# Optimization experiments

Hardware: AMD Instinct MI355X
Metric: run time of the kernel (lower is better)

## Reference

```python
import jax, jax.numpy as jnp
import numpy as np

B, T, C = 512, 256, 384
HEAD = 64

def setup_inputs() -> dict:
    key = jax.random.key(0)
    k1, k2, k3, k4 = jax.random.split(key, 4)
    x = jax.random.normal(k1, (B, T, C), dtype=jnp.float32)
    Wq = jax.random.normal(k2, (C, HEAD), dtype=jnp.float32) * (C ** -0.5)
    Wk = jax.random.normal(k3, (C, HEAD), dtype=jnp.float32) * (C ** -0.5)
    Wv = jax.random.normal(k4, (C, HEAD), dtype=jnp.float32) * (C ** -0.5)
    return {"x": x, "Wq": Wq, "Wk": Wk, "Wv": Wv}

def reference(x, Wq, Wk, Wv):
    # projections (Linear with bias=False): x @ W
    q = jnp.einsum('btc,ch->bth', x, Wq)   # [B,T,H]
    k = jnp.einsum('btc,ch->bth', x, Wk)   # [B,T,H]
    v = jnp.einsum('btc,ch->bth', x, Wv)   # [B,T,H]
    Cdim = x.shape[-1]
    # NOTE: original scales by C**-0.5 where C = nEmbd (not headSize)
    scores = jnp.einsum('bth,bsh->bts', q, k) * (Cdim ** -0.5)  # [B,T,T]
    Tlen = x.shape[1]
    causal = jnp.tril(jnp.ones((Tlen, Tlen), dtype=bool))
    scores = jnp.where(causal, scores, -jnp.inf)
    wei = jax.nn.softmax(scores, axis=-1)
    # dropout omitted (eval mode / deterministic reference)
    out = jnp.einsum('bts,bsh->bth', wei, v)  # [B,T,H]
    return out
```

## Files before the change

### kernel.cpp

```cpp
#include <hip/hip_runtime.h>

#define B_ 512
#define T_ 256
#define C_ 384
#define H_ 64

typedef __bf16 bf16;
typedef bf16  bf16x8 __attribute__((ext_vector_type(8)));
typedef bf16  bf16x2 __attribute__((ext_vector_type(2)));
typedef float f32x4  __attribute__((ext_vector_type(4)));
typedef int   i32x4  __attribute__((ext_vector_type(4)));

#define NCHUNK     3
#define CHUNK_K    128
#define WT3_CHUNK  24576
#define WT3_TOTAL  (NCHUNK * WT3_CHUNK)

__global__ void prep_wt3(const float* __restrict__ Wq,
                         const float* __restrict__ Wk,
                         const float* __restrict__ Wv,
                         bf16* __restrict__ wt3)
{
    int idx = blockIdx.x * 256 + threadIdx.x;
    if (idx >= WT3_TOTAL) return;
    int chunk = idx / WT3_CHUNK;
    int rem   = idx % WT3_CHUNK;
    int s     = rem >> 3;
    int e     = rem & 7;
    int mc    = s >> 4;
    int kkc   = (s & 15) ^ (mc & 7);
    int mat   = mc >> 6;
    int col   = mc & 63;
    int k     = chunk * CHUNK_K + kkc * 8 + e;
    const float* W = (mat == 0) ? Wq : (mat == 1) ? Wk : Wv;
    wt3[idx] = (bf16)W[k * H_ + col];
}

__device__ __forceinline__ bf16x8 cvt8(float4 a, float4 b)
{
    bf16x8 r;
    r[0] = (bf16)a.x; r[1] = (bf16)a.y; r[2] = (bf16)a.z; r[3] = (bf16)a.w;
    r[4] = (bf16)b.x; r[5] = (bf16)b.y; r[6] = (bf16)b.z; r[7] = (bf16)b.w;
    return r;
}

__device__ __forceinline__ unsigned pack2(float a, float b)
{
    bf16x2 v; v[0] = (bf16)a; v[1] = (bf16)b;
    return __builtin_bit_cast(unsigned, v);
}

__device__ __forceinline__ void gload_lds16(const bf16* g, bf16* l)
{
    __builtin_amdgcn_global_load_lds(
        (const __attribute__((address_space(1))) void*)g,
        (__attribute__((address_space(3))) void*)l,
        16, 0, 0);
}

#define SWZ(row, col) ((col) ^ (((row) & 7) << 3))

__device__ __forceinline__ const bf16x8* wts_frag(const bf16* wt_s, int mc, int kk)
{
    int byte = ((mc * CHUNK_K + kk) * 2) ^ ((mc & 7) << 4);
    return reinterpret_cast<const bf16x8*>(reinterpret_cast<const char*>(wt_s) + byte);
}

template<int USE_WT>
__global__ __launch_bounds__(512, 2)
void head_fused12(const float* __restrict__ x,
                  const float* __restrict__ Wq,
                  const float* __restrict__ Wk,
                  const float* __restrict__ Wv,
                  const bf16* __restrict__ wt3,
                  float* __restrict__ out)
{
    __shared__ bf16 lds_u[32768];
    __shared__ bf16 p_s[8 * 16 * 64];

    bf16* wt_s = lds_u;
    bf16* k_s  = lds_u;
    bf16* vT_s = lds_u + 16384;

    const int tid  = threadIdx.x;
    const int wave = tid >> 6;
    const int lane = tid & 63;
    const int lr   = lane & 15;
    const int lg   = lane >> 4;

    const int b = blockIdx.x;
    const float* xb = x + (size_t)b * T_ * C_;
    bf16* pw = &p_s[wave * 16 * 64];

    const int mt0 = wave, mt1 = 15 - wave;
    bf16x8 qf[2][2];

    f32x4 acc[2][3][4];
    #pragma unroll
    for (int t = 0; t < 2; ++t)
        #pragma unroll
        for (int a = 0; a < 3; ++a)
            #pragma unroll
            for (int nw = 0; nw < 4; ++nw)
                acc[t][a][nw] = (f32x4){0.f, 0.f, 0.f, 0.f};

    #pragma unroll 1
    for (int chunk = 0; chunk < NCHUNK; ++chunk) {
        if (chunk) __syncthreads();
        if (USE_WT) {
            #pragma unroll
            for (int c = 0; c < 6; ++c) {
                const bf16* g = wt3 + chunk * WT3_CHUNK + (c * 512 + tid) * 8;
                bf16* l = wt_s + (c * 512 + wave * 64) * 8;
                gload_lds16(g, l);
            }
        } else {
            #pragma unroll
            for (int c = 0; c < 6; ++c) {
                int f16 = c * 512 + tid;
                int mc  = f16 >> 4;
                int kkc = f16 & 15;
                int mat = mc >> 6, col = mc & 63;
                const float* W = (mat == 0) ? Wq : (mat == 1) ? Wk : Wv;
                bf16x8 vv;
                #pragma unroll
                for (int j = 0; j < 8; ++j)
                    vv[j] = (bf16)W[(chunk * CHUNK_K + kkc * 8 + j) * H_ + col];
                int byte = ((mc * CHUNK_K + kkc * 8) * 2) ^ ((mc & 7) << 4);
                *reinterpret_cast<bf16x8*>(reinterpret_cast<char*>(wt_s) + byte) = vv;
            }
        }
        __syncthreads();

        const float* xr0 = xb + (mt0 * 16 + lr) * C_ + chunk * CHUNK_K + lg * 8;
        const float* xr1 = xb + (mt1 * 16 + lr) * C_ + chunk * CHUNK_K + lg * 8;
        #pragma unroll
        for (int ks = 0; ks < 4; ++ks) {
            float4 a0 = *reinterpret_cast<const float4*>(xr0 + ks * 32);
            float4 a1 = *reinterpret_cast<const float4*>(xr0 + ks * 32 + 4);
            float4 b0 = *reinterpret_cast<const float4*>(xr1 + ks * 32);
            float4 b1 = *reinterpret_cast<const float4*>(xr1 + ks * 32 + 4);
            bf16x8 af0 = cvt8(a0, a1);
            bf16x8 af1 = cvt8(b0, b1);
            const int kk = ks * 32 + lg * 8;
            #pragma unroll
            for (int mat = 0; mat < 3; ++mat) {
                #pragma unroll
                for (int nw = 0; nw < 4; ++nw) {
                    bf16x8 bfr = *wts_frag(wt_s, mat * 64 + nw * 16 + lr, kk);
                    acc[0][mat][nw] = __builtin_amdgcn_mfma_f32_16x16x32_bf16(
                        af0, bfr, acc[0][mat][nw], 0, 0, 0);
                    acc[1][mat][nw] = __builtin_amdgcn_mfma_f32_16x16x32_bf16(
                        af1, bfr, acc[1][mat][nw], 0, 0, 0);
                }
            }
        }
    }
    __syncthreads();

    #pragma unroll
    for (int tile = 0; tile < 2; ++tile) {
        const int mt = tile ? mt1 : mt0;
        #pragma unroll
        for (int nw = 0; nw < 4; ++nw) {
            #pragma unroll
            for (int r = 0; r < 4; ++r) {
                int row = mt * 16 + lg * 4 + r;
                int col = nw * 16 + lr;
                k_s[row * 64 + SWZ(row, col)]   = (bf16)acc[tile][1][nw][r];
                vT_s[col * 256 + SWZ(col, row)] = (bf16)acc[tile][2][nw][r];
            }
        }
        #pragma unroll
        for (int nw = 0; nw < 4; ++nw) {
            #pragma unroll
            for (int r = 0; r < 4; ++r) {
                int row = lg * 4 + r;
                pw[row * 64 + SWZ(row, nw * 16 + lr)] = (bf16)acc[tile][0][nw][r];
            }
        }
        asm volatile("s_waitcnt lgkmcnt(0)" ::: "memory");
        __builtin_amdgcn_sched_barrier(0);
        qf[tile][0] = *reinterpret_cast<const bf16x8*>(&pw[lr * 64 + SWZ(lr, lg * 8)]);
        qf[tile][1] = *reinterpret_cast<const bf16x8*>(&pw[lr * 64 + SWZ(lr, 32 + lg * 8)]);
        asm volatile("s_waitcnt lgkmcnt(0)" ::: "memory");
        __builtin_amdgcn_sched_barrier(0);
    }
    __syncthreads();

    const float scale = 0.051031036307982884f;

    #pragma unroll
    for (int p = 0; p < 2; ++p) {
        const int mt  = p ? mt1 : mt0;
        const int nkt = mt + 1;

        float m = -1e30f, l = 0.f;
        f32x4 oacc[4];
        #pragma unroll
        for (int n = 0; n < 4; ++n) oacc[n] = (f32x4){0.f, 0.f, 0.f, 0.f};

        #pragma unroll
        for (int h = 0; h < 2; ++h) {
            const int vh = (nkt - h * 8) < 8 ? (nkt - h * 8) : 8;
            if (vh > 0) {
                float s[8][4];
                #pragma unroll
                for (int j = 0; j < 8; ++j) {
                    const int kt = h * 8 + j;
                    if (j < vh) {
                        bf16x8 kf0 = *reinterpret_cast<const bf16x8*>(
                            &k_s[(kt * 16 + lr) * 64 + SWZ(lr, lg * 8)]);
                        bf16x8 kf1 = *reinterpret_cast<const bf16x8*>(
                            &k_s[(kt * 16 + lr) * 64 + SWZ(lr, 32 + lg * 8)]);
                        f32x4 sc = (f32x4){0.f, 0.f, 0.f, 0.f};
                        sc = __builtin_amdgcn_mfma_f32_16x16x32_bf16(kf0, qf[p][0], sc, 0, 0, 0);
                        sc = __builtin_amdgcn_mfma_f32_16x16x32_bf16(kf1, qf[p][1], sc, 0, 0, 0);
                        #pragma unroll
                        for (int r = 0; r < 4; ++r) {
                            float v = sc[r] * scale;
                            if (kt == mt && (lg * 4 + r) > lr) v = -1e30f;
                            s[j][r] = v;
                        }
                    } else {
                        #pragma unroll
                        for (int r = 0; r < 4; ++r) s[j][r] = -1e30f;
                    }
                }

                float pm = s[0][0];
                #pragma unroll
                for (int j = 0; j < 8; ++j)
                    #pragma unroll
                    for (int r = 0; r < 4; ++r) pm = fmaxf(pm, s[j][r]);
                pm = fmaxf(pm, __shfl_xor(pm, 16));
                pm = fmaxf(pm, __shfl_xor(pm, 32));
                float nm = fmaxf(m, pm);
                float fr = __expf(m - nm);
                m = nm;
                l *= fr;
                #pragma unroll
                for (int n = 0; n < 4; ++n)
                    #pragma unroll
                    for (int r = 0; r < 4; ++r) oacc[n][r] *= fr;

                float tt = 0.f;
                #pragma unroll
                for (int j = 0; j < 8; ++j)
                    #pragma unroll
                    for (int r = 0; r < 4; ++r) {
                        float e = __expf(s[j][r] - m);
                        s[j][r] = e;
                        tt += e;
                    }
                tt += __shfl_xor(tt, 16);
                tt += __shfl_xor(tt, 32);
                l += tt;

                const int nkk = (vh + 1) >> 1;
                #pragma unroll
                for (int kkl = 0; kkl < 4; ++kkl) {
                    if (kkl < nkk) {
                        const int kk = h * 4 + kkl;
                        unsigned lo0 = pack2(s[2*kkl][0],   s[2*kkl][1]);
                        unsigned hi0 = pack2(s[2*kkl][2],   s[2*kkl][3]);
                        unsigned lo1 = pack2(s[2*kkl+1][0], s[2*kkl+1][1]);
                        unsigned hi1 = pack2(s[2*kkl+1][2], s[2*kkl+1][3]);
                        const int src0 = (lg & 1) * 32 + lr;
                        const int src1 = src0 + 16;
                        const bool t1  = (lg >> 1) != 0;
                        int a0 = __shfl((int)lo0, src0), a1 = __shfl((int)lo1, src0);
                        unsigned w0 = t1 ? (unsigned)a1 : (unsigned)a0;
                        int b0 = __shfl((int)hi0, src0), b1 = __shfl((int)hi1, src0);
                        unsigned w1 = t1 ? (unsigned)b1 : (unsigned)b0;
                        int c0 = __shfl((int)lo0, src1), c1 = __shfl((int)lo1, src1);
                        unsigned w2 = t1 ? (unsigned)c1 : (unsigned)c0;
                        int d0 = __shfl((int)hi0, src1), d1 = __shfl((int)hi1, src1);
                        unsigned w3 = t1 ? (unsigned)d1 : (unsigned)d0;
                        i32x4 wi = {(int)w0, (int)w1, (int)w2, (int)w3};
                        bf16x8 pf = __builtin_bit_cast(bf16x8, wi);
                        #pragma unroll
                        for (int n = 0; n < 4; ++n) {
                            bf16x8 vf = *reinterpret_cast<const bf16x8*>(
                                &vT_s[(n * 16 + lr) * 256 + SWZ(lr, kk * 32 + lg * 8)]);
                            oacc[n] = __builtin_amdgcn_mfma_f32_16x16x32_bf16(vf, pf, oacc[n], 0, 0, 0);
                        }
                    }
                }
            }
        }

        const float rin = 1.0f / l;
        float* op = out + ((size_t)b * T_ + mt * 16 + lr) * H_;
        #pragma unroll
        for (int n = 0; n < 4; ++n) {
            float4 st;
            st.x = oacc[n][0] * rin;
            st.y = oacc[n][1] * rin;
            st.z = oacc[n][2] * rin;
            st.w = oacc[n][3] * rin;
            *reinterpret_cast<float4*>(op + n * 16 + lg * 4) = st;
        }
    }
}

extern "C" void kernel_launch(void* const* d_in, const int* in_sizes, int n_in,
                              void* d_out, int out_size, void* d_ws, size_t ws_size,
                              hipStream_t stream)
{
    (void)in_sizes; (void)n_in; (void)out_size;
    const float* x  = (const float*)d_in[0];
    const float* Wq = (const float*)d_in[1];
    const float* Wk = (const float*)d_in[2];
    const float* Wv = (const float*)d_in[3];
    float* o = (float*)d_out;

    if (ws_size >= (size_t)(WT3_TOTAL * sizeof(bf16))) {
        bf16* wt3 = (bf16*)d_ws;
        prep_wt3<<<dim3((WT3_TOTAL + 255) / 256), dim3(256), 0, stream>>>(Wq, Wk, Wv, wt3);
        head_fused12<1><<<dim3(B_), dim3(512), 0, stream>>>(x, Wq, Wk, Wv, wt3, o);
    } else {
        head_fused12<0><<<dim3(B_), dim3(512), 0, stream>>>(x, Wq, Wk, Wv, nullptr, o);
    }
}
```

Before: 64.91 us.

## Double-buffer weight chunks in LDS to overlap staging with projection MFMAs

Splits the K dimension of the QKV projection into six 64-wide chunks and ping-pongs two LDS weight buffers. The next chunk's weight load is issued before the current chunk's MFMAs, so global-to-LDS traffic overlaps compute. This removes one of the two barriers per chunk. In exchange there are twice as many chunk iterations and barriers, and the x reads per iteration are smaller.

```diff
diff --git a/kernel.cpp b/kernel.cpp
--- a/kernel.cpp
+++ b/kernel.cpp
@@ -11,9 +11,9 @@
 typedef float f32x4  __attribute__((ext_vector_type(4)));
 typedef int   i32x4  __attribute__((ext_vector_type(4)));
 
-#define NCHUNK     3
-#define CHUNK_K    128
-#define WT3_CHUNK  24576
+#define NCHUNK     6
+#define CHUNK_K    64
+#define WT3_CHUNK  12288
 #define WT3_TOTAL  (NCHUNK * WT3_CHUNK)
 
 __global__ void prep_wt3(const float* __restrict__ Wq,
@@ -27,8 +27,8 @@
     int rem   = idx % WT3_CHUNK;
     int s     = rem >> 3;
     int e     = rem & 7;
-    int mc    = s >> 4;
-    int kkc   = (s & 15) ^ (mc & 7);
+    int mc    = s >> 3;
+    int kkc   = (s & 7) ^ (mc & 7);
     int mat   = mc >> 6;
     int col   = mc & 63;
     int k     = chunk * CHUNK_K + kkc * 8 + e;
@@ -60,15 +60,15 @@
 
 #define SWZ(row, col) ((col) ^ (((row) & 7) << 3))
 
-__device__ __forceinline__ const bf16x8* wts_frag(const bf16* wt_s, int mc, int kk)
+__device__ __forceinline__ const bf16x8* wts_frag(const bf16* buf, int mc, int kk)
 {
     int byte = ((mc * CHUNK_K + kk) * 2) ^ ((mc & 7) << 4);
-    return reinterpret_cast<const bf16x8*>(reinterpret_cast<const char*>(wt_s) + byte);
+    return reinterpret_cast<const bf16x8*>(reinterpret_cast<const char*>(buf) + byte);
 }
 
 template<int USE_WT>
 __global__ __launch_bounds__(512, 2)
-void head_fused12(const float* __restrict__ x,
+void head_fused13(const float* __restrict__ x,
                   const float* __restrict__ Wq,
                   const float* __restrict__ Wk,
                   const float* __restrict__ Wv,
@@ -78,7 +78,8 @@
     __shared__ bf16 lds_u[32768];
     __shared__ bf16 p_s[8 * 16 * 64];
 
-    bf16* wt_s = lds_u;
+    bf16* wtb0 = lds_u;
+    bf16* wtb1 = lds_u + WT3_CHUNK;
     bf16* k_s  = lds_u;
     bf16* vT_s = lds_u + 16384;
 
@@ -104,22 +105,20 @@
             for (int nw = 0; nw < 4; ++nw)
                 acc[t][a][nw] = (f32x4){0.f, 0.f, 0.f, 0.f};
 
-    #pragma unroll 1
-    for (int chunk = 0; chunk < NCHUNK; ++chunk) {
-        if (chunk) __syncthreads();
+    auto stage_chunk = [&](int chunk, bf16* buf) {
         if (USE_WT) {
             #pragma unroll
-            for (int c = 0; c < 6; ++c) {
+            for (int c = 0; c < 3; ++c) {
                 const bf16* g = wt3 + chunk * WT3_CHUNK + (c * 512 + tid) * 8;
-                bf16* l = wt_s + (c * 512 + wave * 64) * 8;
+                bf16* l = buf + (c * 512 + wave * 64) * 8;
                 gload_lds16(g, l);
             }
         } else {
             #pragma unroll
-            for (int c = 0; c < 6; ++c) {
-                int f16 = c * 512 + tid;
-                int mc  = f16 >> 4;
-                int kkc = f16 & 15;
+            for (int c = 0; c < 3; ++c) {
+                int s   = c * 512 + tid;
+                int mc  = s >> 3;
+                int kkc = (s & 7);
                 int mat = mc >> 6, col = mc & 63;
                 const float* W = (mat == 0) ? Wq : (mat == 1) ? Wk : Wv;
                 bf16x8 vv;
@@ -127,27 +126,42 @@
                 for (int j = 0; j < 8; ++j)
                     vv[j] = (bf16)W[(chunk * CHUNK_K + kkc * 8 + j) * H_ + col];
                 int byte = ((mc * CHUNK_K + kkc * 8) * 2) ^ ((mc & 7) << 4);
-                *reinterpret_cast<bf16x8*>(reinterpret_cast<char*>(wt_s) + byte) = vv;
-            }
-        }
-        __syncthreads();
+                *reinterpret_cast<bf16x8*>(reinterpret_cast<char*>(buf) + byte) = vv;
+            }
+        }
+    };
+
+    stage_chunk(0, wtb0);
+    __syncthreads();
+
+    #pragma unroll 2
+    for (int chunk = 0; chunk < NCHUNK; ++chunk) {
+        bf16* cur = (chunk & 1) ? wtb1 : wtb0;
+        bf16* nxt = (chunk & 1) ? wtb0 : wtb1;
 
         const float* xr0 = xb + (mt0 * 16 + lr) * C_ + chunk * CHUNK_K + lg * 8;
         const float* xr1 = xb + (mt1 * 16 + lr) * C_ + chunk * CHUNK_K + lg * 8;
-        #pragma unroll
-        for (int ks = 0; ks < 4; ++ks) {
-            float4 a0 = *reinterpret_cast<const float4*>(xr0 + ks * 32);
-            float4 a1 = *reinterpret_cast<const float4*>(xr0 + ks * 32 + 4);
-            float4 b0 = *reinterpret_cast<const float4*>(xr1 + ks * 32);
-            float4 b1 = *reinterpret_cast<const float4*>(xr1 + ks * 32 + 4);
-            bf16x8 af0 = cvt8(a0, a1);
-            bf16x8 af1 = cvt8(b0, b1);
+        float4 a0 = *reinterpret_cast<const float4*>(xr0);
+        float4 a1 = *reinterpret_cast<const float4*>(xr0 + 4);
+        float4 a2 = *reinterpret_cast<const float4*>(xr0 + 32);
+        float4 a3 = *reinterpret_cast<const float4*>(xr0 + 36);
+        float4 b0 = *reinterpret_cast<const float4*>(xr1);
+        float4 b1 = *reinterpret_cast<const float4*>(xr1 + 4);
+        float4 b2 = *reinterpret_cast<const float4*>(xr1 + 32);
+        float4 b3 = *reinterpret_cast<const float4*>(xr1 + 36);
+
+        if (chunk < NCHUNK - 1) stage_chunk(chunk + 1, nxt);
+
+        #pragma unroll
+        for (int ks = 0; ks < 2; ++ks) {
+            bf16x8 af0 = (ks == 0) ? cvt8(a0, a1) : cvt8(a2, a3);
+            bf16x8 af1 = (ks == 0) ? cvt8(b0, b1) : cvt8(b2, b3);
             const int kk = ks * 32 + lg * 8;
             #pragma unroll
             for (int mat = 0; mat < 3; ++mat) {
                 #pragma unroll
                 for (int nw = 0; nw < 4; ++nw) {
-                    bf16x8 bfr = *wts_frag(wt_s, mat * 64 + nw * 16 + lr, kk);
+                    bf16x8 bfr = *wts_frag(cur, mat * 64 + nw * 16 + lr, kk);
                     acc[0][mat][nw] = __builtin_amdgcn_mfma_f32_16x16x32_bf16(
                         af0, bfr, acc[0][mat][nw], 0, 0, 0);
                     acc[1][mat][nw] = __builtin_amdgcn_mfma_f32_16x16x32_bf16(
@@ -155,8 +169,8 @@
                 }
             }
         }
+        __syncthreads();
     }
-    __syncthreads();
 
     #pragma unroll
     for (int tile = 0; tile < 2; ++tile) {
@@ -318,8 +332,8 @@
     if (ws_size >= (size_t)(WT3_TOTAL * sizeof(bf16))) {
         bf16* wt3 = (bf16*)d_ws;
         prep_wt3<<<dim3((WT3_TOTAL + 255) / 256), dim3(256), 0, stream>>>(Wq, Wk, Wv, wt3);
-        head_fused12<1><<<dim3(B_), dim3(512), 0, stream>>>(x, Wq, Wk, Wv, wt3, o);
+        head_fused13<1><<<dim3(B_), dim3(512), 0, stream>>>(x, Wq, Wk, Wv, wt3, o);
     } else {
-        head_fused12<0><<<dim3(B_), dim3(512), 0, stream>>>(x, Wq, Wk, Wv, nullptr, o);
+        head_fused13<0><<<dim3(B_), dim3(512), 0, stream>>>(x, Wq, Wk, Wv, nullptr, o);
     }
 }
```

Measured after the change: 66.40 us. 1.02x slower.
